# Kernel optimization log

Measured on AMD Instinct MI355X. Metric: run time of the kernel, lower is better.

## Reference

```python
import jax, jax.numpy as jnp
import numpy as np

N_HEAD, N_KV, HEAD_DIM, GATE_CH = 16, 4, 128, 32

def _rope(x, cos, sin):
    d = x.shape[3] // 2
    x1, x2 = x[..., :d], x[..., d:]
    return jnp.concatenate([x1 * cos + x2 * sin, x1 * (-sin) + x2 * cos], axis=3)

def _rmsnorm(x):
    xf = x.astype(jnp.float32)
    return (x * jax.lax.rsqrt(jnp.mean(xf * xf, axis=-1, keepdims=True) + 1e-6)).astype(x.dtype)

def setup_inputs() -> dict:
    key = jax.random.key(0)
    ks = jax.random.split(key, 9)
    B, T, C = 2, 2048, 2048
    return {
        "x":  jax.random.normal(ks[0], (B, T, C), jnp.float32),
        "ve": jax.random.normal(ks[1], (B, T, N_KV * HEAD_DIM), jnp.float32),
        "cos": jax.random.uniform(ks[2], (T, 1, HEAD_DIM // 2), jnp.float32),
        "sin": jax.random.uniform(ks[3], (T, 1, HEAD_DIM // 2), jnp.float32),
        "Wq": jax.random.normal(ks[4], (C, N_HEAD * HEAD_DIM), jnp.float32) * 0.02,
        "Wk": jax.random.normal(ks[5], (C, N_KV * HEAD_DIM), jnp.float32) * 0.02,
        "Wv": jax.random.normal(ks[6], (C, N_KV * HEAD_DIM), jnp.float32) * 0.02,
        "Wg": jax.random.normal(ks[7], (GATE_CH, N_KV), jnp.float32) * 0.02,
        "Wo": jax.random.normal(ks[8], (C, C), jnp.float32) * 0.02,
        "window": 1024,
    }

def reference(x, ve, cos, sin, Wq, Wk, Wv, Wg, Wo, window):
    B, T, C = x.shape
    q = (x @ Wq).reshape(B, T, N_HEAD, HEAD_DIM)
    k = (x @ Wk).reshape(B, T, N_KV, HEAD_DIM)
    v = (x @ Wv).reshape(B, T, N_KV, HEAD_DIM)
    # value-embedding gate (ve_gate active for this layer)
    gate = 2.0 * jax.nn.sigmoid(x[..., :GATE_CH] @ Wg)  # (B,T,N_KV)
    v = v + gate[..., None] * ve.reshape(B, T, N_KV, HEAD_DIM)
    q, k = _rope(q, cos, sin), _rope(k, cos, sin)
    q, k = _rmsnorm(q), _rmsnorm(k)
    # GQA: repeat kv heads (repeat_interleave over head dim)
    groups = N_HEAD // N_KV
    k = jnp.repeat(k, groups, axis=2)
    v = jnp.repeat(v, groups, axis=2)
    scale = 1.0 / np.sqrt(HEAD_DIM)
    scores = jnp.einsum("bthd,bshd->bhts", q, k) * scale  # (B,H,T,T)
    idx = jnp.arange(T)
    diff = idx[None, :] - idx[:, None]  # diff[i,j] = j - i, as in torch code
    mask = (diff >= 0) & (diff < window)
    scores = jnp.where(mask[None, None], scores, -jnp.inf)
    p = jax.nn.softmax(scores, axis=-1)
    y = jnp.einsum("bhts,bshd->bthd", p, v).reshape(B, T, C)
    return y @ Wo
```

## Files before the change

### kernel.cpp

```cpp
#include <hip/hip_runtime.h>
#include <hip/hip_bf16.h>
#include <cstdint>

typedef __hip_bfloat16 bf16;
typedef __attribute__((ext_vector_type(8))) short short8;
typedef __attribute__((ext_vector_type(4))) short short4v;
typedef __attribute__((ext_vector_type(4))) float f32x4;

#define T_   2048
#define CDIM 2048
#define NH   16
#define NKV  4
#define HD   128
#define QSCALE (0.08838834764831845f * 1.44269504088896340f)

__device__ __forceinline__ void gload_lds16(const void* g, void* l) {
  __builtin_amdgcn_global_load_lds(
      (const __attribute__((address_space(1))) void*)g,
      (__attribute__((address_space(3))) void*)l, 16, 0, 0);
}

template <int G> __device__ __forceinline__ void vm_gate() {
  if constexpr (G == 6)      asm volatile("s_waitcnt vmcnt(6)" ::: "memory");
  else if constexpr (G == 5) asm volatile("s_waitcnt vmcnt(5)" ::: "memory");
  else                       asm volatile("s_waitcnt vmcnt(0)" ::: "memory");
}

__global__ __launch_bounds__(256) void prep_kernel(
    const float* __restrict__ x, const float* __restrict__ Wq,
    const float* __restrict__ Wk, const float* __restrict__ Wv,
    const float* __restrict__ Wo, ushort4* __restrict__ xb,
    bf16* __restrict__ wT, bf16* __restrict__ woT) {
  int b = blockIdx.x;
  if (b < 8192) {
    int i = b * 256 + threadIdx.x;
    float4 v = ((const float4*)x)[i];
    union { bf16 h[4]; ushort4 u; } cv;
    cv.h[0] = __float2bfloat16(v.x);
    cv.h[1] = __float2bfloat16(v.y);
    cv.h[2] = __float2bfloat16(v.z);
    cv.h[3] = __float2bfloat16(v.w);
    xb[i] = cv.u;
    return;
  }
  const float* W; bf16* WT; int N, nbx, idx;
  if (b < 12288)      { W = Wq; WT = wT;                       N = 2048; nbx = 64; idx = b - 8192; }
  else if (b < 13312) { W = Wk; WT = wT + (size_t)2048 * 2048; N = 512;  nbx = 16; idx = b - 12288; }
  else if (b < 14336) { W = Wv; WT = wT + (size_t)2560 * 2048; N = 512;  nbx = 16; idx = b - 13312; }
  else                { W = Wo; WT = woT;                      N = 2048; nbx = 64; idx = b - 14336; }
  __shared__ float tile[32][33];
  const int K = 2048;
  int n0 = (idx % nbx) * 32, k0 = (idx / nbx) * 32;
  int r = threadIdx.x >> 5, c = threadIdx.x & 31;
  for (int i = 0; i < 4; ++i)
    tile[r + i * 8][c] = W[(size_t)(k0 + r + i * 8) * N + n0 + c];
  __syncthreads();
  for (int i = 0; i < 4; ++i)
    WT[(size_t)(n0 + r + i * 8) * K + k0 + c] = __float2bfloat16(tile[c][r + i * 8]);
}

template <int MREP, int NREP, typename CT>
__global__ __launch_bounds__(512, 2) void gemm_pp(const bf16* __restrict__ A,
                                                  const bf16* __restrict__ BT,
                                                  CT* __restrict__ C,
                                                  int N, int K, int RY, int RX) {
  constexpr int BM = MREP * 32;
  constexpr int BN = NREP * 64;
  constexpr int QN = (MREP == 8) ? 4 : 2;
  constexpr int MI = MREP / 4;
  constexpr int GATE = NREP + QN - 1;
  __shared__ __align__(16) bf16 sA[2][BM * 64];
  __shared__ __align__(16) bf16 sB[2][BN * 64];

  int tid = threadIdx.x;
  int lane = tid & 63, w = tid >> 6;
  int wm = w >> 2, wn = w & 3;
  int lr = lane & 15, lk = lane >> 4;

  int xcd = blockIdx.x & 7, t = blockIdx.x >> 3;
  int by = (xcd >> 1) * RY + t / RX;
  int bx = (xcd & 1) * RX + t % RX;
  int m0 = by * BM, n0 = bx * BN;

  f32x4 acc[MREP][NREP];
#pragma unroll
  for (int m = 0; m < MREP; ++m)
#pragma unroll
    for (int n = 0; n < NREP; ++n) acc[m][n] = (f32x4){0.f, 0.f, 0.f, 0.f};

  const bf16* Abase = A + (size_t)m0 * K;
  const bf16* Bbase = BT + (size_t)n0 * K;

  auto stageB = [&](int p, int kt) {
    int kb = kt << 6;
#pragma unroll
    for (int i = 0; i < NREP; ++i) {
      int c = i * 512 + tid;
      int r = c >> 3, sl = c & 7;
      gload_lds16(Bbase + (size_t)r * K + kb + ((sl ^ (r & 7)) << 3),
                  (char*)(&sB[p][0]) + c * 16);
    }
  };
  auto stageAq = [&](int p, int kt, int q) {
    int kb = kt << 6;
    int rbase = 32 * q + ((w & 3) << 3) + ((w >> 2) * (BM / 2));
    int r = rbase + (lane >> 3), sl = lane & 7;
    gload_lds16(Abase + (size_t)r * K + kb + ((sl ^ (r & 7)) << 3),
                (char*)(&sA[p][0]) + rbase * 128 + lane * 16);
  };

  int nk = K >> 6;
  stageB(0, 0);
#pragma unroll
  for (int q = 0; q < QN; ++q) stageAq(0, 0, q);
  stageB(1, 1);
#pragma unroll
  for (int q = 0; q < QN - 1; ++q) stageAq(1, 1, q);
  vm_gate<GATE>();
  __builtin_amdgcn_s_barrier();

#define READ_A_FRAGS(PH)                                                   \
  {                                                                        \
    _Pragma("unroll")                                                      \
    for (int mi = 0; mi < MI; ++mi) {                                      \
      int row = wm * (MREP * 16) + ((PH) * MI + mi) * 16 + lr;             \
      const char* rb = sAb + row * 128;                                    \
      int rx = (row & 7) << 4;                                             \
      af[mi][0] = *(const short8*)(rb + ((lk * 16) ^ rx));                 \
      af[mi][1] = *(const short8*)(rb + ((64 + lk * 16) ^ rx));            \
    }                                                                      \
  }
#define MFMA_PH(PH)                                                        \
  __builtin_amdgcn_s_setprio(1);                                           \
  _Pragma("unroll")                                                        \
  for (int kk = 0; kk < 2; ++kk)                                           \
    _Pragma("unroll")                                                      \
    for (int mi = 0; mi < MI; ++mi)                                        \
      _Pragma("unroll")                                                    \
      for (int n = 0; n < NREP; ++n)                                       \
        acc[(PH) * MI + mi][n] = __builtin_amdgcn_mfma_f32_16x16x32_bf16(  \
            af[mi][kk], bfr[n][kk], acc[(PH) * MI + mi][n], 0, 0, 0);      \
  __builtin_amdgcn_s_setprio(0);
#define LGKM_FENCE                                                         \
  asm volatile("s_waitcnt lgkmcnt(0)" ::: "memory");                       \
  __builtin_amdgcn_sched_barrier(0);

  for (int kt = 0; kt < nk; ++kt) {
    int p = kt & 1;
    const char* sAb = (const char*)(&sA[p][0]);
    const char* sBb = (const char*)(&sB[p][0]);
    short8 bfr[NREP][2], af[MI][2];

#pragma unroll
    for (int n = 0; n < NREP; ++n) {
      int row = wn * (NREP * 16) + n * 16 + lr;
      const char* rb = sBb + row * 128;
      int rx = (row & 7) << 4;
      bfr[n][0] = *(const short8*)(rb + ((lk * 16) ^ rx));
      bfr[n][1] = *(const short8*)(rb + ((64 + lk * 16) ^ rx));
    }
    READ_A_FRAGS(0);
    if (kt + 1 < nk) stageAq(p ^ 1, kt + 1, QN - 1);
    LGKM_FENCE;
    MFMA_PH(0);
    __builtin_amdgcn_s_barrier();

    READ_A_FRAGS(1);
    if (kt + 2 < nk) {
      stageB(p, kt + 2);
      if constexpr (QN == 4) stageAq(p, kt + 2, 0);
    }
    LGKM_FENCE;
    MFMA_PH(1);
    __builtin_amdgcn_s_barrier();

    READ_A_FRAGS(2);
    if (kt + 2 < nk) stageAq(p, kt + 2, (QN == 4) ? 1 : 0);
    LGKM_FENCE;
    MFMA_PH(2);
    __builtin_amdgcn_s_barrier();

    READ_A_FRAGS(3);
    if constexpr (QN == 4) {
      if (kt + 2 < nk) stageAq(p, kt + 2, 2);
    }
    LGKM_FENCE;
    MFMA_PH(3);
    if (kt + 2 < nk) vm_gate<GATE>();
    else             vm_gate<0>();
    __builtin_amdgcn_s_barrier();
  }
#undef READ_A_FRAGS
#undef MFMA_PH
#undef LGKM_FENCE

#pragma unroll
  for (int m = 0; m < MREP; ++m)
#pragma unroll
    for (int n = 0; n < NREP; ++n)
#pragma unroll
      for (int jj = 0; jj < 4; ++jj) {
        size_t idx = (size_t)(m0 + wm * (MREP * 16) + m * 16 + lk * 4 + jj) * N +
                     n0 + wn * (NREP * 16) + n * 16 + lr;
        if constexpr (__is_same(CT, float))
          C[idx] = acc[m][n][jj];
        else
          C[idx] = __float2bfloat16(acc[m][n][jj]);
      }
}

__global__ __launch_bounds__(256) void epilogue_kernel(
    const bf16* __restrict__ qkv, const float* __restrict__ x,
    const float* __restrict__ ve, const float* __restrict__ cosT,
    const float* __restrict__ sinT, const float* __restrict__ Wg,
    bf16* __restrict__ qn, bf16* __restrict__ kn, bf16* __restrict__ vT) {
  int row = blockIdx.x;
  int bi = row >> 11, t = row & 2047;
  int tid = threadIdx.x, lane = tid & 63, w = tid >> 6;
  __shared__ float gate[NKV];
  size_t rb = (size_t)row * 3072;

  if (tid < 128) {
    int g = tid >> 5, i = tid & 31;
    float p = x[(size_t)row * CDIM + i] * Wg[i * 4 + g];
    p += __shfl_xor(p, 1);  p += __shfl_xor(p, 2);
    p += __shfl_xor(p, 4);  p += __shfl_xor(p, 8);
    p += __shfl_xor(p, 16);
    if (i == 0) gate[g] = 2.f / (1.f + __expf(-p));
  }
  __syncthreads();

  float cv = cosT[t * 64 + lane];
  float sv = sinT[t * 64 + lane];

  for (int it = 0; it < 4; ++it) {
    int h = it * 4 + w;
    float x1 = __bfloat162float(qkv[rb + h * 128 + lane]);
    float x2 = __bfloat162float(qkv[rb + h * 128 + 64 + lane]);
    float y1 = x1 * cv + x2 * sv;
    float y2 = x2 * cv - x1 * sv;
    float ss = y1 * y1 + y2 * y2;
    ss += __shfl_xor(ss, 1);  ss += __shfl_xor(ss, 2);  ss += __shfl_xor(ss, 4);
    ss += __shfl_xor(ss, 8);  ss += __shfl_xor(ss, 16); ss += __shfl_xor(ss, 32);
    float r = rsqrtf(ss * (1.f / 128.f) + 1e-6f) * QSCALE;
    size_t ob = (size_t)row * (NH * HD) + h * 128;
    qn[ob + lane] = __float2bfloat16(y1 * r);
    qn[ob + 64 + lane] = __float2bfloat16(y2 * r);
  }
  {
    int h = w;
    float x1 = __bfloat162float(qkv[rb + 2048 + h * 128 + lane]);
    float x2 = __bfloat162float(qkv[rb + 2048 + h * 128 + 64 + lane]);
    float y1 = x1 * cv + x2 * sv;
    float y2 = x2 * cv - x1 * sv;
    float ss = y1 * y1 + y2 * y2;
    ss += __shfl_xor(ss, 1);  ss += __shfl_xor(ss, 2);  ss += __shfl_xor(ss, 4);
    ss += __shfl_xor(ss, 8);  ss += __shfl_xor(ss, 16); ss += __shfl_xor(ss, 32);
    float r = rsqrtf(ss * (1.f / 128.f) + 1e-6f);
    size_t ob = (size_t)row * (NKV * HD) + h * 128;
    kn[ob + lane] = __float2bfloat16(y1 * r);
    kn[ob + 64 + lane] = __float2bfloat16(y2 * r);
  }
  for (int e = tid; e < 512; e += 256) {
    int kv = e >> 7, d = e & 127;
    float val = __bfloat162float(qkv[rb + 2560 + e]) + gate[kv] * ve[(size_t)row * 512 + e];
    vT[((size_t)(bi * NKV + kv) * HD + d) * T_ + t] = __float2bfloat16(val);
  }
}

__global__ __launch_bounds__(256, 2) void attn_kernel(
    const bf16* __restrict__ qn, const bf16* __restrict__ kn,
    const bf16* __restrict__ vT, bf16* __restrict__ y,
    const int* __restrict__ winp) {
  __shared__ __align__(16) bf16 sK[2][64 * 128];
  __shared__ __align__(16) bf16 sV[2][128 * 64];

  int win = *winp;
  int id = blockIdx.x;
  int g  = id & 7;
  int bi = g >> 2, kvh = g & 3;
  int rem = id >> 3;
  int h  = kvh * 4 + (rem & 3);
  int q0 = (rem >> 2) << 7;
  int tid = threadIdx.x;
  int lane = tid & 63, w = tid >> 6;
  int lr = lane & 15, lk = lane >> 4;

  short8 qfA[4], qfB[4];
  {
    const bf16* qrA = qn + (size_t)(bi * T_ + q0 + w * 32 + lr) * (NH * HD) + h * HD;
    const bf16* qrB = qrA + (size_t)16 * (NH * HD);
#pragma unroll
    for (int c = 0; c < 4; ++c) {
      qfA[c] = *(const short8*)(qrA + c * 32 + lk * 8);
      qfB[c] = *(const short8*)(qrB + c * 32 + lk * 8);
    }
  }

  int kge[4], klb[4], vge[4], vlbA[4], vlbB[4];
#pragma unroll
  for (int i = 0; i < 4; ++i) {
    int c = i * 256 + tid;
    int kr = c >> 4, ks = c & 15;
    kge[i] = kr * (NKV * HD) + ks * 8;
    klb[i] = kr * 256 + ((ks ^ (kr & 7)) << 4);
    int vr = c >> 3, vs = c & 7;
    vge[i] = vr * T_ + vs * 8;
    int hh = vs >> 2, m = vs & 3, a = m >> 1;
    int sA = 8 * ((2 * m) & 3) + 4 * a;
    int sB = 8 * ((2 * m + 1) & 3) + 4 * a;
    int tA = 64 * hh + 2 * sA, tB = 64 * hh + 2 * sB;
    vlbA[i] = vr * 128 + (((tA >> 4) ^ (vr & 7)) << 4) + (tA & 15);
    vlbB[i] = vr * 128 + (((tB >> 4) ^ (vr & 7)) << 4) + (tB & 15);
  }
  const bf16* kpane = kn + (size_t)bi * T_ * (NKV * HD) + kvh * HD;
  const bf16* vpane = vT + (size_t)(bi * NKV + kvh) * HD * T_;

  short8 kreg[4], vreg[4];
  auto LOAD = [&](int jtx) {
    const bf16* kb = kpane + (size_t)(jtx << 6) * (NKV * HD);
    const bf16* vb = vpane + (jtx << 6);
#pragma unroll
    for (int i = 0; i < 4; ++i) kreg[i] = *(const short8*)(kb + kge[i]);
#pragma unroll
    for (int i = 0; i < 4; ++i) vreg[i] = *(const short8*)(vb + vge[i]);
  };
  auto WRITE = [&](int b) {
    char* kBuf = (char*)(&sK[b][0]);
    char* vBuf = (char*)(&sV[b][0]);
#pragma unroll
    for (int i = 0; i < 4; ++i) *(short8*)(kBuf + klb[i]) = kreg[i];
#pragma unroll
    for (int i = 0; i < 4; ++i) {
      union { short8 s8; short4v s4[2]; } u;
      u.s8 = vreg[i];
      *(short4v*)(vBuf + vlbA[i]) = u.s4[0];
      *(short4v*)(vBuf + vlbB[i]) = u.s4[1];
    }
  };

  f32x4 o0[8], o1[8];
#pragma unroll
  for (int i = 0; i < 8; ++i) {
    o0[i] = (f32x4){0.f, 0.f, 0.f, 0.f};
    o1[i] = (f32x4){0.f, 0.f, 0.f, 0.f};
  }
  float lp0 = 0.f, lp1 = 0.f;

  int jt0 = q0 >> 6;
  int hi = q0 + 126 + win; if (hi > T_ - 1) hi = T_ - 1;
  int jt1 = hi >> 6;

  LOAD(jt0);
  WRITE(0);
  if (jt0 < jt1) LOAD(jt0 + 1);
  asm volatile("s_waitcnt lgkmcnt(0)\n\ts_barrier" ::: "memory");

  int irow0 = q0 + w * 32 + lr;
  int klo = lk * 4;

  int p = 0;
  for (int jt = jt0; jt <= jt1; ++jt) {
    int j0 = jt << 6;

    if (jt < jt1) {
      WRITE(p ^ 1);
      if (jt + 1 < jt1) LOAD(jt + 2);
    }

    const char* sKb = (const char*)(&sK[p][0]);
    const char* sVb = (const char*)(&sV[p][0]);

    f32x4 s0[4], s1[4];
#pragma unroll
    for (int sub = 0; sub < 4; ++sub) {
      s0[sub] = (f32x4){0.f, 0.f, 0.f, 0.f};
      s1[sub] = (f32x4){0.f, 0.f, 0.f, 0.f};
    }
    __builtin_amdgcn_s_setprio(1);
#pragma unroll
    for (int sub = 0; sub < 4; ++sub) {
      int kr = sub * 16 + lr;
      int rx = (kr & 7) << 4;
      const char* rowb = sKb + kr * 256;
#pragma unroll
      for (int c = 0; c < 4; ++c) {
        short8 kf = *(const short8*)(rowb + ((c * 64 + lk * 16) ^ rx));
        s0[sub] = __builtin_amdgcn_mfma_f32_16x16x32_bf16(kf, qfA[c], s0[sub], 0, 0, 0);
        s1[sub] = __builtin_amdgcn_mfma_f32_16x16x32_bf16(kf, qfB[c], s1[sub], 0, 0, 0);
      }
    }
    __builtin_amdgcn_s_setprio(0);

    bool full = (j0 >= q0 + 128) && (j0 + 64 <= q0 + win);
    int koff0 = j0 - irow0;
    int koff1 = koff0 - 16;

    short8 pA0, pA1, pB0, pB1;
    {
      unsigned pk[8];
#pragma unroll
      for (int sub = 0; sub < 4; ++sub) {
        float p0 = exp2f(s0[sub][0]), p1 = exp2f(s0[sub][1]);
        float p2 = exp2f(s0[sub][2]), p3 = exp2f(s0[sub][3]);
        if (!full) {
          int base = koff0 + sub * 16 + klo;
          p0 = ((unsigned)(base + 0) < (unsigned)win) ? p0 : 0.f;
          p1 = ((unsigned)(base + 1) < (unsigned)win) ? p1 : 0.f;
          p2 = ((unsigned)(base + 2) < (unsigned)win) ? p2 : 0.f;
          p3 = ((unsigned)(base + 3) < (unsigned)win) ? p3 : 0.f;
        }
        lp0 += (p0 + p1) + (p2 + p3);
        asm("v_cvt_pk_bf16_f32 %0, %1, %2" : "=v"(pk[sub * 2])     : "v"(p0), "v"(p1));
        asm("v_cvt_pk_bf16_f32 %0, %1, %2" : "=v"(pk[sub * 2 + 1]) : "v"(p2), "v"(p3));
      }
      union { unsigned u[4]; short8 s8; } c0, c1;
      c0.u[0] = pk[0]; c0.u[1] = pk[1]; c0.u[2] = pk[2]; c0.u[3] = pk[3];
      c1.u[0] = pk[4]; c1.u[1] = pk[5]; c1.u[2] = pk[6]; c1.u[3] = pk[7];
      pA0 = c0.s8; pA1 = c1.s8;
    }
    {
      unsigned pk[8];
#pragma unroll
      for (int sub = 0; sub < 4; ++sub) {
        float p0 = exp2f(s1[sub][0]), p1 = exp2f(s1[sub][1]);
        float p2 = exp2f(s1[sub][2]), p3 = exp2f(s1[sub][3]);
        if (!full) {
          int base = koff1 + sub * 16 + klo;
          p0 = ((unsigned)(base + 0) < (unsigned)win) ? p0 : 0.f;
          p1 = ((unsigned)(base + 1) < (unsigned)win) ? p1 : 0.f;
          p2 = ((unsigned)(base + 2) < (unsigned)win) ? p2 : 0.f;
          p3 = ((unsigned)(base + 3) < (unsigned)win) ? p3 : 0.f;
        }
        lp1 += (p0 + p1) + (p2 + p3);
        asm("v_cvt_pk_bf16_f32 %0, %1, %2" : "=v"(pk[sub * 2])     : "v"(p0), "v"(p1));
        asm("v_cvt_pk_bf16_f32 %0, %1, %2" : "=v"(pk[sub * 2 + 1]) : "v"(p2), "v"(p3));
      }
      union { unsigned u[4]; short8 s8; } c0, c1;
      c0.u[0] = pk[0]; c0.u[1] = pk[1]; c0.u[2] = pk[2]; c0.u[3] = pk[3];
      c1.u[0] = pk[4]; c1.u[1] = pk[5]; c1.u[2] = pk[6]; c1.u[3] = pk[7];
      pB0 = c0.s8; pB1 = c1.s8;
    }

    __builtin_amdgcn_s_setprio(1);
#pragma unroll
    for (int nb = 0; nb < 8; ++nb) {
      int vr = nb * 16 + lr;
      int vrx = (vr & 7) << 4;
      const char* vb = sVb + vr * 128;
      short8 vf0 = *(const short8*)(vb + ((lk * 16) ^ vrx));
      short8 vf1 = *(const short8*)(vb + ((64 + lk * 16) ^ vrx));
      o0[nb] = __builtin_amdgcn_mfma_f32_16x16x32_bf16(pA0, vf0, o0[nb], 0, 0, 0);
      o0[nb] = __builtin_amdgcn_mfma_f32_16x16x32_bf16(pA1, vf1, o0[nb], 0, 0, 0);
      o1[nb] = __builtin_amdgcn_mfma_f32_16x16x32_bf16(pB0, vf0, o1[nb], 0, 0, 0);
      o1[nb] = __builtin_amdgcn_mfma_f32_16x16x32_bf16(pB1, vf1, o1[nb], 0, 0, 0);
    }
    __builtin_amdgcn_s_setprio(0);

    asm volatile("s_waitcnt lgkmcnt(0)\n\ts_barrier" ::: "memory");
    p ^= 1;
  }

  float l0 = lp0, l1 = lp1;
  l0 += __shfl_xor(l0, 16); l0 += __shfl_xor(l0, 32);
  l1 += __shfl_xor(l1, 16); l1 += __shfl_xor(l1, 32);
#pragma unroll
  for (int jj = 0; jj < 4; ++jj) {
    float inv0 = 1.f / __shfl(l0, klo + jj);
    float inv1 = 1.f / __shfl(l1, klo + jj);
    size_t ob0 = (size_t)(bi * T_ + q0 + w * 32 + klo + jj) * (NH * HD) + h * HD;
    size_t ob1 = ob0 + (size_t)16 * (NH * HD);
#pragma unroll
    for (int nb = 0; nb < 8; ++nb) {
      y[ob0 + nb * 16 + lr] = __float2bfloat16(o0[nb][jj] * inv0);
      y[ob1 + nb * 16 + lr] = __float2bfloat16(o1[nb][jj] * inv1);
    }
  }
}

extern "C" void kernel_launch(void* const* d_in, const int* in_sizes, int n_in,
                              void* d_out, int out_size, void* d_ws, size_t ws_size,
                              hipStream_t stream) {
  const float* x    = (const float*)d_in[0];
  const float* ve   = (const float*)d_in[1];
  const float* cosT = (const float*)d_in[2];
  const float* sinT = (const float*)d_in[3];
  const float* Wq   = (const float*)d_in[4];
  const float* Wk   = (const float*)d_in[5];
  const float* Wv   = (const float*)d_in[6];
  const float* Wg   = (const float*)d_in[7];
  const float* Wo   = (const float*)d_in[8];
  const int*   win  = (const int*)d_in[9];
  float* out = (float*)d_out;

  char* ws = (char*)d_ws;
  bf16*  xb   = (bf16*)(ws);
  bf16*  wT   = (bf16*)(ws + 16777216);
  bf16*  woT  = (bf16*)(ws + 29360128);
  bf16*  qkvb = (bf16*)(ws + 37748736);
  bf16*  qn   = (bf16*)(ws + 62914560);
  bf16*  kn   = (bf16*)(ws + 79691776);
  bf16*  vTb  = (bf16*)(ws + 83886080);
  bf16*  y    = qkvb;

  prep_kernel<<<18432, 256, 0, stream>>>(x, Wq, Wk, Wv, Wo, (ushort4*)xb, wT, woT);

  gemm_pp<8, 3, bf16><<<256, 512, 0, stream>>>(xb, wT, qkvb, 3072, 2048, 4, 8);
  epilogue_kernel<<<4096, 256, 0, stream>>>(qkvb, x, ve, cosT, sinT, Wg, qn, kn, vTb);
  attn_kernel<<<512, 256, 0, stream>>>(qn, kn, vTb, y, win);
  gemm_pp<4, 4, float><<<256, 512, 0, stream>>>(y, woT, out, 2048, 2048, 8, 4);
}
```

Before: 187.4 us.

## Restructure GEMM into quadrant-ordered MFMA schedule with 256-row A tiles

Replaces the templated ping-pong GEMM with a version fixed at 256-row A tiles whose per-iteration work is split into four MFMA quadrants, so A and B register fragments are reused across quadrants. A and B loads for later k-steps are issued as half-tiles interleaved between quadrants, and each phase starts with a barrier. The output projection GEMM now uses 256x128 tiles instead of 128x256, with a matching grid remap. The aim is fewer LDS reads and better overlap of global-to-LDS traffic with MFMA, at the cost of more barriers and higher register pressure.

```diff
diff --git a/kernel.cpp b/kernel.cpp
--- a/kernel.cpp
+++ b/kernel.cpp
@@ -21,8 +21,8 @@
 }
 
 template <int G> __device__ __forceinline__ void vm_gate() {
-  if constexpr (G == 6)      asm volatile("s_waitcnt vmcnt(6)" ::: "memory");
-  else if constexpr (G == 5) asm volatile("s_waitcnt vmcnt(5)" ::: "memory");
+  if constexpr (G == 5)      asm volatile("s_waitcnt vmcnt(5)" ::: "memory");
+  else if constexpr (G == 4) asm volatile("s_waitcnt vmcnt(4)" ::: "memory");
   else                       asm volatile("s_waitcnt vmcnt(0)" ::: "memory");
 }
 
@@ -59,17 +59,15 @@
     WT[(size_t)(n0 + r + i * 8) * K + k0 + c] = __float2bfloat16(tile[c][r + i * 8]);
 }
 
-template <int MREP, int NREP, typename CT>
-__global__ __launch_bounds__(512, 2) void gemm_pp(const bf16* __restrict__ A,
+template <int NF, typename CT>
+__global__ __launch_bounds__(512, 2) void gemm_q4(const bf16* __restrict__ A,
                                                   const bf16* __restrict__ BT,
                                                   CT* __restrict__ C,
                                                   int N, int K, int RY, int RX) {
-  constexpr int BM = MREP * 32;
-  constexpr int BN = NREP * 64;
-  constexpr int QN = (MREP == 8) ? 4 : 2;
-  constexpr int MI = MREP / 4;
-  constexpr int GATE = NREP + QN - 1;
-  __shared__ __align__(16) bf16 sA[2][BM * 64];
+  constexpr int BN = NF * 64;
+  constexpr int NB0 = (NF + 1) / 2;
+  constexpr int NB1 = NF - NB0;
+  __shared__ __align__(16) bf16 sA[2][256 * 64];
   __shared__ __align__(16) bf16 sB[2][BN * 64];
 
   int tid = threadIdx.x;
@@ -80,68 +78,81 @@
   int xcd = blockIdx.x & 7, t = blockIdx.x >> 3;
   int by = (xcd >> 1) * RY + t / RX;
   int bx = (xcd & 1) * RX + t % RX;
-  int m0 = by * BM, n0 = bx * BN;
-
-  f32x4 acc[MREP][NREP];
-#pragma unroll
-  for (int m = 0; m < MREP; ++m)
-#pragma unroll
-    for (int n = 0; n < NREP; ++n) acc[m][n] = (f32x4){0.f, 0.f, 0.f, 0.f};
+  int m0 = by * 256, n0 = bx * BN;
+
+  f32x4 acc[8][NF];
+#pragma unroll
+  for (int m = 0; m < 8; ++m)
+#pragma unroll
+    for (int n = 0; n < NF; ++n) acc[m][n] = (f32x4){0.f, 0.f, 0.f, 0.f};
 
   const bf16* Abase = A + (size_t)m0 * K;
   const bf16* Bbase = BT + (size_t)n0 * K;
 
-  auto stageB = [&](int p, int kt) {
+  auto stB = [&](int p, int kt) {
     int kb = kt << 6;
 #pragma unroll
-    for (int i = 0; i < NREP; ++i) {
+    for (int i = 0; i < NF; ++i) {
       int c = i * 512 + tid;
       int r = c >> 3, sl = c & 7;
       gload_lds16(Bbase + (size_t)r * K + kb + ((sl ^ (r & 7)) << 3),
                   (char*)(&sB[p][0]) + c * 16);
     }
   };
-  auto stageAq = [&](int p, int kt, int q) {
+  auto stA = [&](int p, int kt, int h) {
     int kb = kt << 6;
-    int rbase = 32 * q + ((w & 3) << 3) + ((w >> 2) * (BM / 2));
-    int r = rbase + (lane >> 3), sl = lane & 7;
-    gload_lds16(Abase + (size_t)r * K + kb + ((sl ^ (r & 7)) << 3),
-                (char*)(&sA[p][0]) + rbase * 128 + lane * 16);
+#pragma unroll
+    for (int i = 0; i < 2; ++i) {
+      int c = i * 512 + tid;
+      int r = (c >> 3) + h * 128, sl = c & 7;
+      gload_lds16(Abase + (size_t)r * K + kb + ((sl ^ (r & 7)) << 3),
+                  (char*)(&sA[p][0]) + r * 128 + sl * 16);
+    }
   };
 
   int nk = K >> 6;
-  stageB(0, 0);
-#pragma unroll
-  for (int q = 0; q < QN; ++q) stageAq(0, 0, q);
-  stageB(1, 1);
-#pragma unroll
-  for (int q = 0; q < QN - 1; ++q) stageAq(1, 1, q);
-  vm_gate<GATE>();
+  stB(0, 0); stA(0, 0, 0); stA(0, 0, 1);
+  stB(1, 1); stA(1, 1, 0);
+  vm_gate<NF + 2>();
   __builtin_amdgcn_s_barrier();
 
-#define READ_A_FRAGS(PH)                                                   \
+#define READ_AF(DST, QM)                                                   \
   {                                                                        \
     _Pragma("unroll")                                                      \
-    for (int mi = 0; mi < MI; ++mi) {                                      \
-      int row = wm * (MREP * 16) + ((PH) * MI + mi) * 16 + lr;             \
+    for (int mi = 0; mi < 4; ++mi) {                                       \
+      int row = wm * 128 + (QM) * 64 + mi * 16 + lr;                       \
       const char* rb = sAb + row * 128;                                    \
       int rx = (row & 7) << 4;                                             \
-      af[mi][0] = *(const short8*)(rb + ((lk * 16) ^ rx));                 \
-      af[mi][1] = *(const short8*)(rb + ((64 + lk * 16) ^ rx));            \
+      DST[mi][0] = *(const short8*)(rb + ((lk * 16) ^ rx));                \
+      DST[mi][1] = *(const short8*)(rb + ((64 + lk * 16) ^ rx));           \
     }                                                                      \
   }
-#define MFMA_PH(PH)                                                        \
+#define READ_BF(DST, FBASE, CNT)                                           \
+  {                                                                        \
+    _Pragma("unroll")                                                      \
+    for (int f = 0; f < (CNT); ++f) {                                      \
+      int row = wn * (NF * 16) + ((FBASE) + f) * 16 + lr;                  \
+      const char* rb = sBb + row * 128;                                    \
+      int rx = (row & 7) << 4;                                             \
+      DST[f][0] = *(const short8*)(rb + ((lk * 16) ^ rx));                 \
+      DST[f][1] = *(const short8*)(rb + ((64 + lk * 16) ^ rx));            \
+    }                                                                      \
+  }
+#define MFMA_Q(AF, BF, QM, FBASE, CNT)                                     \
   __builtin_amdgcn_s_setprio(1);                                           \
   _Pragma("unroll")                                                        \
   for (int kk = 0; kk < 2; ++kk)                                           \
     _Pragma("unroll")                                                      \
-    for (int mi = 0; mi < MI; ++mi)                                        \
+    for (int mi = 0; mi < 4; ++mi)                                         \
       _Pragma("unroll")                                                    \
-      for (int n = 0; n < NREP; ++n)                                       \
-        acc[(PH) * MI + mi][n] = __builtin_amdgcn_mfma_f32_16x16x32_bf16(  \
-            af[mi][kk], bfr[n][kk], acc[(PH) * MI + mi][n], 0, 0, 0);      \
+      for (int f = 0; f < (CNT); ++f)                                      \
+        acc[(QM) * 4 + mi][(FBASE) + f] =                                  \
+            __builtin_amdgcn_mfma_f32_16x16x32_bf16(                       \
+                AF[mi][kk], BF[f][kk], acc[(QM) * 4 + mi][(FBASE) + f],    \
+                0, 0, 0);                                                  \
   __builtin_amdgcn_s_setprio(0);
-#define LGKM_FENCE                                                         \
+#define RD_SYNC                                                            \
+  __builtin_amdgcn_s_barrier();                                            \
   asm volatile("s_waitcnt lgkmcnt(0)" ::: "memory");                       \
   __builtin_amdgcn_sched_barrier(0);
 
@@ -149,59 +160,46 @@
     int p = kt & 1;
     const char* sAb = (const char*)(&sA[p][0]);
     const char* sBb = (const char*)(&sB[p][0]);
-    short8 bfr[NREP][2], af[MI][2];
-
-#pragma unroll
-    for (int n = 0; n < NREP; ++n) {
-      int row = wn * (NREP * 16) + n * 16 + lr;
-      const char* rb = sBb + row * 128;
-      int rx = (row & 7) << 4;
-      bfr[n][0] = *(const short8*)(rb + ((lk * 16) ^ rx));
-      bfr[n][1] = *(const short8*)(rb + ((64 + lk * 16) ^ rx));
-    }
-    READ_A_FRAGS(0);
-    if (kt + 1 < nk) stageAq(p ^ 1, kt + 1, QN - 1);
-    LGKM_FENCE;
-    MFMA_PH(0);
+    short8 af0[4][2], af1[4][2], bf0[NB0][2], bf1[NB1][2];
+
+    READ_AF(af0, 0);
+    READ_BF(bf0, 0, NB0);
+    if (kt + 1 < nk) stA(p ^ 1, kt + 1, 1);
+    RD_SYNC;
+    MFMA_Q(af0, bf0, 0, 0, NB0);
     __builtin_amdgcn_s_barrier();
 
-    READ_A_FRAGS(1);
-    if (kt + 2 < nk) {
-      stageB(p, kt + 2);
-      if constexpr (QN == 4) stageAq(p, kt + 2, 0);
-    }
-    LGKM_FENCE;
-    MFMA_PH(1);
+    READ_BF(bf1, NB0, NB1);
+    RD_SYNC;
+    MFMA_Q(af0, bf1, 0, NB0, NB1);
     __builtin_amdgcn_s_barrier();
 
-    READ_A_FRAGS(2);
-    if (kt + 2 < nk) stageAq(p, kt + 2, (QN == 4) ? 1 : 0);
-    LGKM_FENCE;
-    MFMA_PH(2);
+    READ_AF(af1, 1);
+    if (kt + 2 < nk) stB(p, kt + 2);
+    RD_SYNC;
+    MFMA_Q(af1, bf1, 1, NB0, NB1);
     __builtin_amdgcn_s_barrier();
 
-    READ_A_FRAGS(3);
-    if constexpr (QN == 4) {
-      if (kt + 2 < nk) stageAq(p, kt + 2, 2);
-    }
-    LGKM_FENCE;
-    MFMA_PH(3);
-    if (kt + 2 < nk) vm_gate<GATE>();
+    if (kt + 2 < nk) stA(p, kt + 2, 0);
+    MFMA_Q(af1, bf0, 1, 0, NB0);
+    if (kt + 2 < nk) vm_gate<NF + 2>();
     else             vm_gate<0>();
     __builtin_amdgcn_s_barrier();
   }
-#undef READ_A_FRAGS
-#undef MFMA_PH
-#undef LGKM_FENCE
-
-#pragma unroll
-  for (int m = 0; m < MREP; ++m)
-#pragma unroll
-    for (int n = 0; n < NREP; ++n)
+#undef READ_AF
+#undef READ_BF
+#undef MFMA_Q
+#undef RD_SYNC
+
+#pragma unroll
+  for (int m = 0; m < 8; ++m)
+#pragma unroll
+    for (int n = 0; n < NF; ++n)
 #pragma unroll
       for (int jj = 0; jj < 4; ++jj) {
-        size_t idx = (size_t)(m0 + wm * (MREP * 16) + m * 16 + lk * 4 + jj) * N +
-                     n0 + wn * (NREP * 16) + n * 16 + lr;
+        size_t idx = (size_t)(m0 + wm * 128 + (m >> 2) * 64 + (m & 3) * 16 +
+                              lk * 4 + jj) * N +
+                     n0 + wn * (NF * 16) + n * 16 + lr;
         if constexpr (__is_same(CT, float))
           C[idx] = acc[m][n][jj];
         else
@@ -505,8 +503,8 @@
 
   prep_kernel<<<18432, 256, 0, stream>>>(x, Wq, Wk, Wv, Wo, (ushort4*)xb, wT, woT);
 
-  gemm_pp<8, 3, bf16><<<256, 512, 0, stream>>>(xb, wT, qkvb, 3072, 2048, 4, 8);
+  gemm_q4<3, bf16><<<256, 512, 0, stream>>>(xb, wT, qkvb, 3072, 2048, 4, 8);
   epilogue_kernel<<<4096, 256, 0, stream>>>(qkvb, x, ve, cosT, sinT, Wg, qn, kn, vTb);
   attn_kernel<<<512, 256, 0, stream>>>(qn, kn, vTb, y, win);
-  gemm_pp<4, 4, float><<<256, 512, 0, stream>>>(y, woT, out, 2048, 2048, 8, 4);
-}
+  gemm_q4<2, float><<<256, 512, 0, stream>>>(y, woT, out, 2048, 2048, 4, 8);
+}
```

New measurement: 178.2 us (median of 2 runs). -4.9%, faster.
